# Kernel tuning notes

Measured on AMD Instinct MI355X. Metric: run time of the kernel, lower is better.

Reference implementation:

```python
import jax, jax.numpy as jnp
import numpy as np

MESSAGE_SIZE = 128
MESSAGE_PASSES = 3
N_BONDS = 7      # Single, Double, Triple, Quadruple, Aromatic, Pi, Universal
N_LAYERS = 8     # 8 bias-free Linear layers, ReLU after the first 7
N_TYPES = 6      # top-4 ranked atoms + atom 0, plus catchall slot (index 5)
ATOM_VALS = [6.0, 7.0, 8.0, 9.0, 16.0, 17.0, 1.0]
TOP_ATOMS = [6.0, 7.0, 8.0, 9.0, 0.0]


def setup_inputs() -> dict:
    key = jax.random.key(0)
    ks = jax.random.split(key, 8)
    B, N, F, D = 128, 128, 75, MESSAGE_SIZE
    g = jax.random.uniform(ks[0], (B, N_BONDS, N, N), dtype=jnp.float32)
    h = jax.random.normal(ks[1], (B, N, F), dtype=jnp.float32)
    # channel 0 carries the atomic number used for GRU routing
    atom_ids = jax.random.randint(ks[2], (B, N), 0, len(ATOM_VALS))
    h = h.at[:, :, 0].set(jnp.asarray(ATOM_VALS, jnp.float32)[atom_ids])
    s = 1.0 / np.sqrt(D)
    msg_W = jax.random.normal(ks[3], (N_BONDS, N_LAYERS, D, D), jnp.float32) * s
    gru_Wih = jax.random.normal(ks[4], (2, N_TYPES, 3 * D, D), jnp.float32) * s  # [regular/universal, type, 3H, H]
    gru_Whh = jax.random.normal(ks[5], (2, N_TYPES, 3 * D, D), jnp.float32) * s
    gru_bih = jax.random.normal(ks[6], (2, N_TYPES, 3 * D), jnp.float32) * s
    gru_bhh = jax.random.normal(ks[7], (2, N_TYPES, 3 * D), jnp.float32) * s
    return dict(g=g, h=h, msg_W=msg_W, gru_Wih=gru_Wih, gru_Whh=gru_Whh,
                gru_bih=gru_bih, gru_bhh=gru_bhh)


def _gru_grouped(x, hx, tid, Wih, Whh, bih, bhh):
    """torch.nn.GRUCell(input=x, hx=hx) with per-node parameter group tid in [0,T).
    Wih/Whh: [T, 3H, H], bih/bhh: [T, 3H]."""
    gx = jnp.einsum('nd,tgd->ntg', x, Wih)   # [n, T, 3H]
    gh = jnp.einsum('nd,tgd->ntg', hx, Whh)
    gx = jnp.take_along_axis(gx, tid[:, None, None], axis=1)[:, 0] + bih[tid]
    gh = jnp.take_along_axis(gh, tid[:, None, None], axis=1)[:, 0] + bhh[tid]
    xr, xz, xn = jnp.split(gx, 3, axis=-1)
    hr, hz, hn = jnp.split(gh, 3, axis=-1)
    r = jax.nn.sigmoid(xr + hr)
    z = jax.nn.sigmoid(xz + hz)
    n = jnp.tanh(xn + r * hn)
    return (1.0 - z) * n + z * hx


def reference(g, h, msg_W, gru_Wih, gru_Whh, gru_bih, gru_bhh):
    B, N, F = h.shape
    D = msg_W.shape[-1]
    h_t = jnp.concatenate([h, jnp.zeros((B, N, D - F), h.dtype)], axis=2)  # [B,N,D]
    atoms = h[:, :, 0].reshape(-1)
    tid = jnp.full(atoms.shape, N_TYPES - 1, jnp.int32)  # default catchall
    for i, a in enumerate(TOP_ATOMS):
        tid = jnp.where(atoms == jnp.float32(a), jnp.int32(i), tid)
    for _ in range(MESSAGE_PASSES):
        # per-bond-type 8-layer bias-free MLP, vectorized over the 7 bond types
        xb = jnp.broadcast_to(h_t[None], (N_BONDS, B, N, D))
        for l in range(N_LAYERS):
            xb = jnp.einsum('kbnd,ked->kbne', xb, msg_W[:, l])
            if l < N_LAYERS - 1:
                xb = jax.nn.relu(xb)
        # bmm aggregation per bond type: m_k = g[:,k] @ xb_k
        m_all = jnp.einsum('bknm,kbmd->kbnd', g, xb)
        m_non = m_all[:N_BONDS - 1].sum(0).reshape(-1, D)
        m_uni = m_all[N_BONDS - 1].reshape(-1, D)
        h_flat = h_t.reshape(-1, D)
        out = _gru_grouped(h_flat, m_non, tid, gru_Wih[0], gru_Whh[0], gru_bih[0], gru_bhh[0])
        out_u = _gru_grouped(h_flat, m_uni, tid, gru_Wih[1], gru_Whh[1], gru_bih[1], gru_bhh[1])
        h_t = (out + out_u).reshape(B, N, D)
    return h_t
```

## Files before the change

kernel.cpp:

```cpp
#include <hip/hip_runtime.h>
#include <math.h>

#define NBOND 7
#define NLAY 8
#define NTYPE 6
#define NNODES 16384
#define PX 136

typedef _Float16 half8 __attribute__((ext_vector_type(8)));
typedef _Float16 half4 __attribute__((ext_vector_type(4)));
typedef float floatx16 __attribute__((ext_vector_type(16)));

__device__ __forceinline__ float sig_(float x) { return 1.0f / (1.0f + __expf(-x)); }
__device__ __forceinline__ int drow_(int reg, int hi) { return (reg & 3) + 8 * (reg >> 2) + 4 * hi; }

__device__ __forceinline__ _Float16 hi_(float v) { return (_Float16)v; }
__device__ __forceinline__ _Float16 lo_(float v) { return (_Float16)(v - (float)(_Float16)v); }

__global__ void setup_kernel(const float* __restrict__ h, float* __restrict__ hT,
                             int* __restrict__ counts, int* __restrict__ bucket)
{
    int gid = blockIdx.x * 256 + threadIdx.x;
    int node = gid >> 7, d = gid & 127;
    hT[gid] = (d < 75) ? h[node * 75 + d] : 0.0f;
    if (gid < NNODES) {
        float a = h[gid * 75];
        int tt = 5;
        if      (a == 6.0f) tt = 0;
        else if (a == 7.0f) tt = 1;
        else if (a == 8.0f) tt = 2;
        else if (a == 9.0f) tt = 3;
        else if (a == 0.0f) tt = 4;
        int slot = atomicAdd(&counts[tt], 1);
        bucket[tt * NNODES + slot] = gid;
    }
}

__global__ void pack_msg_kernel(const float* __restrict__ msgW, _Float16* __restrict__ Wp)
{
    int idx = blockIdx.x * 256 + threadIdx.x;
    if (idx >= NBOND * NLAY * 16 * 128) return;
    int e  = idx & 127;
    int c  = (idx >> 7) & 15;
    int kl = idx >> 11;
    const float* src = msgW + ((size_t)kl * 128 + e) * 128 + c * 8;
    float4 u = *(const float4*)src;
    float4 v = *(const float4*)(src + 4);
    float av[8] = {u.x, u.y, u.z, u.w, v.x, v.y, v.z, v.w};
    half8 hh, ll;
    #pragma unroll
    for (int j = 0; j < 8; ++j) { hh[j] = hi_(av[j]); ll[j] = lo_(av[j]); }
    _Float16* dst = Wp + ((size_t)kl * 16 + c) * 2048;
    *(half8*)(dst + e * 8)        = hh;
    *(half8*)(dst + 1024 + e * 8) = ll;
}

__global__ void pack_gru_kernel(const float* __restrict__ Wih, const float* __restrict__ Whh,
                                _Float16* __restrict__ Wp)
{
    int idx = blockIdx.x * 256 + threadIdx.x;
    if (idx >= 2 * NTYPE * 2 * 16 * 384) return;
    int col = idx % 384;
    int c   = (idx / 384) & 15;
    int vm  = idx / 6144;
    int mat = vm & 1;
    int vt  = vm >> 1;
    const float* src = (mat ? Whh : Wih) + ((size_t)vt * 384 + col) * 128 + c * 8;
    float4 u = *(const float4*)src;
    float4 v = *(const float4*)(src + 4);
    float av[8] = {u.x, u.y, u.z, u.w, v.x, v.y, v.z, v.w};
    half8 hh, ll;
    #pragma unroll
    for (int j = 0; j < 8; ++j) { hh[j] = hi_(av[j]); ll[j] = lo_(av[j]); }
    _Float16* dst = Wp + (size_t)vm * 98304 + (size_t)c * 6144;
    *(half8*)(dst + col * 8)        = hh;
    *(half8*)(dst + 3072 + col * 8) = ll;
}

__global__ __launch_bounds__(512, 4) void mlp_agg_mfma(
    const float* __restrict__ hin, const _Float16* __restrict__ Wp,
    const float* __restrict__ gmat, float* __restrict__ m_non, float* __restrict__ m_uni)
{
    __shared__ _Float16 Xhi[128 * PX];
    __shared__ _Float16 Xlo[128 * PX];

    const int t = threadIdx.x;
    const int kb = blockIdx.x, b = blockIdx.y;
    const int wave = t >> 6, lane = t & 63, lo = lane & 31, hi = lane >> 5;
    const int ctw = wave & 3, rh = wave >> 2;
    const int wcol = ctw * 32 + lo;

    for (int q = t; q < 128 * 32; q += 512) {
        int r = q >> 5, c4 = q & 31;
        float4 v = *(const float4*)(hin + ((size_t)(b * 128 + r)) * 128 + c4 * 4);
        half4 hh, ll;
        hh[0] = hi_(v.x); ll[0] = lo_(v.x);
        hh[1] = hi_(v.y); ll[1] = lo_(v.y);
        hh[2] = hi_(v.z); ll[2] = lo_(v.z);
        hh[3] = hi_(v.w); ll[3] = lo_(v.w);
        *(half4*)(Xhi + r * PX + c4 * 4) = hh;
        *(half4*)(Xlo + r * PX + c4 * 4) = ll;
    }
    __syncthreads();

    floatx16 acc[2];

    #pragma unroll 1
    for (int l = 0; l < NLAY; ++l) {
        #pragma unroll
        for (int r2 = 0; r2 < 2; ++r2) acc[r2] = (floatx16)0.0f;
        const _Float16* wb = Wp + ((size_t)(kb * NLAY + l) * 16) * 2048;

        #pragma unroll
        for (int kk = 0; kk < 8; ++kk) {
            const _Float16* bp = wb + (size_t)(kk * 2 + hi) * 2048;
            half8 b_h = *(const half8*)(bp + wcol * 8);
            half8 b_l = *(const half8*)(bp + 1024 + wcol * 8);
            #pragma unroll
            for (int r2 = 0; r2 < 2; ++r2) {
                int rrow = (rh * 2 + r2) * 32 + lo;
                half8 a_h = *(const half8*)(Xhi + rrow * PX + kk * 16 + hi * 8);
                half8 a_l = *(const half8*)(Xlo + rrow * PX + kk * 16 + hi * 8);
                acc[r2] = __builtin_amdgcn_mfma_f32_32x32x16_f16(a_h, b_h, acc[r2], 0, 0, 0);
                acc[r2] = __builtin_amdgcn_mfma_f32_32x32x16_f16(a_h, b_l, acc[r2], 0, 0, 0);
                acc[r2] = __builtin_amdgcn_mfma_f32_32x32x16_f16(a_l, b_h, acc[r2], 0, 0, 0);
            }
        }
        __syncthreads();

        if (l < NLAY - 1) {
            #pragma unroll
            for (int r2 = 0; r2 < 2; ++r2)
                #pragma unroll
                for (int reg = 0; reg < 16; ++reg) {
                    int n = (rh * 2 + r2) * 32 + drow_(reg, hi);
                    float vv = fmaxf(acc[r2][reg], 0.0f);
                    Xhi[n * PX + wcol] = hi_(vv);
                    Xlo[n * PX + wcol] = lo_(vv);
                }
        } else {
            #pragma unroll
            for (int r2 = 0; r2 < 2; ++r2)
                #pragma unroll
                for (int s = 0; s < 4; ++s) {
                    int m0 = (rh * 2 + r2) * 32 + 8 * s + 4 * hi;
                    half4 hh, ll;
                    #pragma unroll
                    for (int j = 0; j < 4; ++j) {
                        float vv = acc[r2][4 * s + j];
                        hh[j] = hi_(vv); ll[j] = lo_(vv);
                    }
                    *(half4*)(Xhi + wcol * PX + m0) = hh;
                    *(half4*)(Xlo + wcol * PX + m0) = ll;
                }
        }
        __syncthreads();
    }

    const int rtw = wave & 3, ch = wave >> 2;
    const int row = rtw * 32 + lo;
    #pragma unroll
    for (int c2 = 0; c2 < 2; ++c2) acc[c2] = (floatx16)0.0f;
    const float* grow = gmat + (size_t)(b * NBOND + kb) * 16384;

    #pragma unroll 2
    for (int kk = 0; kk < 8; ++kk) {
        const float* gp = grow + (size_t)row * 128 + kk * 16 + hi * 8;
        float4 u = *(const float4*)gp, v2 = *(const float4*)(gp + 4);
        float av[8] = {u.x, u.y, u.z, u.w, v2.x, v2.y, v2.z, v2.w};
        half8 a_h, a_l;
        #pragma unroll
        for (int j = 0; j < 8; ++j) { a_h[j] = hi_(av[j]); a_l[j] = lo_(av[j]); }
        #pragma unroll
        for (int c2 = 0; c2 < 2; ++c2) {
            int ct = ch * 2 + c2;
            half8 b_h = *(const half8*)(Xhi + (ct * 32 + lo) * PX + kk * 16 + hi * 8);
            half8 b_l = *(const half8*)(Xlo + (ct * 32 + lo) * PX + kk * 16 + hi * 8);
            acc[c2] = __builtin_amdgcn_mfma_f32_32x32x16_f16(a_h, b_h, acc[c2], 0, 0, 0);
            acc[c2] = __builtin_amdgcn_mfma_f32_32x32x16_f16(a_h, b_l, acc[c2], 0, 0, 0);
            acc[c2] = __builtin_amdgcn_mfma_f32_32x32x16_f16(a_l, b_h, acc[c2], 0, 0, 0);
        }
    }

    if (kb == NBOND - 1) {
        #pragma unroll
        for (int c2 = 0; c2 < 2; ++c2)
            #pragma unroll
            for (int reg = 0; reg < 16; ++reg) {
                int n = rtw * 32 + drow_(reg, hi);
                m_uni[((size_t)(b * 128 + n)) * 128 + (ch * 2 + c2) * 32 + lo] = acc[c2][reg];
            }
    } else {
        #pragma unroll
        for (int c2 = 0; c2 < 2; ++c2)
            #pragma unroll
            for (int reg = 0; reg < 16; ++reg) {
                int n = rtw * 32 + drow_(reg, hi);
                atomicAdd(m_non + ((size_t)(b * 128 + n)) * 128 + (ch * 2 + c2) * 32 + lo,
                          acc[c2][reg]);
            }
    }
}

__global__ __launch_bounds__(256, 3) void gru_mfma(
    float* __restrict__ hT,
    const float* __restrict__ m_non, const float* __restrict__ m_uni,
    const int* __restrict__ counts, const int* __restrict__ bucket,
    const _Float16* __restrict__ Wp, const float* __restrict__ bihp, const float* __restrict__ bhhp)
{
    __shared__ _Float16 Xh[32 * PX], Xl[32 * PX], Mh[32 * PX], Ml[32 * PX];
    __shared__ int bl[32];

    const int t = threadIdx.x, tt = blockIdx.y, rtile = blockIdx.z;
    const int cnt  = counts[tt];
    const int base = blockIdx.x * 64 + rtile * 32;
    if (base >= cnt) return;
    const int nn = min(32, cnt - base);
    if (t < 32) bl[t] = (t < nn) ? bucket[tt * NNODES + base + t] : -1;
    __syncthreads();

    for (int q = t; q < 32 * 32; q += 256) {
        int r = q >> 5, c4 = q & 31;
        float4 xv = make_float4(0.f, 0.f, 0.f, 0.f);
        int node = bl[r];
        if (node >= 0) xv = *(const float4*)(hT + (size_t)node * 128 + c4 * 4);
        half4 hh, ll;
        hh[0] = hi_(xv.x); ll[0] = lo_(xv.x);
        hh[1] = hi_(xv.y); ll[1] = lo_(xv.y);
        hh[2] = hi_(xv.z); ll[2] = lo_(xv.z);
        hh[3] = hi_(xv.w); ll[3] = lo_(xv.w);
        *(half4*)(Xh + r * PX + c4 * 4) = hh;
        *(half4*)(Xl + r * PX + c4 * 4) = ll;
    }

    const int wave = t >> 6, lane = t & 63, lo = lane & 31, hi = lane >> 5;
    const int d = wave * 32 + lo;

    #pragma unroll 1
    for (int v = 0; v < 2; ++v) {
        const float* msrc = v ? m_uni : m_non;
        __syncthreads();
        for (int q = t; q < 32 * 32; q += 256) {
            int r = q >> 5, c4 = q & 31;
            float4 mv = make_float4(0.f, 0.f, 0.f, 0.f);
            int node = bl[r];
            if (node >= 0) mv = *(const float4*)(msrc + (size_t)node * 128 + c4 * 4);
            half4 hh, ll;
            hh[0] = hi_(mv.x); ll[0] = lo_(mv.x);
            hh[1] = hi_(mv.y); ll[1] = lo_(mv.y);
            hh[2] = hi_(mv.z); ll[2] = lo_(mv.z);
            hh[3] = hi_(mv.w); ll[3] = lo_(mv.w);
            *(half4*)(Mh + r * PX + c4 * 4) = hh;
            *(half4*)(Ml + r * PX + c4 * 4) = ll;
        }
        __syncthreads();

        const int vt = v * NTYPE + tt;
        const _Float16* pih = Wp + (size_t)(vt * 2 + 0) * 98304;
        const _Float16* phh = Wp + (size_t)(vt * 2 + 1) * 98304;

        floatx16 ar = (floatx16)0.0f, az = (floatx16)0.0f;
        floatx16 ax = (floatx16)0.0f, ah = (floatx16)0.0f;

        #pragma unroll 2
        for (int kk = 0; kk < 8; ++kk) {
            int koff = kk * 16 + hi * 8;
            half8 xh = *(const half8*)(Xh + lo * PX + koff);
            half8 xl = *(const half8*)(Xl + lo * PX + koff);
            half8 mh = *(const half8*)(Mh + lo * PX + koff);
            half8 ml = *(const half8*)(Ml + lo * PX + koff);
            const _Float16* ci = pih + (size_t)(kk * 2 + hi) * 6144;
            const _Float16* ch = phh + (size_t)(kk * 2 + hi) * 6144;
            half8 birh = *(const half8*)(ci + (0   + d) * 8);
            half8 birl = *(const half8*)(ci + 3072 + (0   + d) * 8);
            half8 bizh = *(const half8*)(ci + (128 + d) * 8);
            half8 bizl = *(const half8*)(ci + 3072 + (128 + d) * 8);
            half8 binh = *(const half8*)(ci + (256 + d) * 8);
            half8 binl = *(const half8*)(ci + 3072 + (256 + d) * 8);
            half8 bhrh = *(const half8*)(ch + (0   + d) * 8);
            half8 bhrl = *(const half8*)(ch + 3072 + (0   + d) * 8);
            half8 bhzh = *(const half8*)(ch + (128 + d) * 8);
            half8 bhzl = *(const half8*)(ch + 3072 + (128 + d) * 8);
            half8 bhnh = *(const half8*)(ch + (256 + d) * 8);
            half8 bhnl = *(const half8*)(ch + 3072 + (256 + d) * 8);

            ar = __builtin_amdgcn_mfma_f32_32x32x16_f16(xh, birh, ar, 0, 0, 0);
            ar = __builtin_amdgcn_mfma_f32_32x32x16_f16(xh, birl, ar, 0, 0, 0);
            ar = __builtin_amdgcn_mfma_f32_32x32x16_f16(xl, birh, ar, 0, 0, 0);
            ar = __builtin_amdgcn_mfma_f32_32x32x16_f16(mh, bhrh, ar, 0, 0, 0);
            ar = __builtin_amdgcn_mfma_f32_32x32x16_f16(mh, bhrl, ar, 0, 0, 0);
            ar = __builtin_amdgcn_mfma_f32_32x32x16_f16(ml, bhrh, ar, 0, 0, 0);

            az = __builtin_amdgcn_mfma_f32_32x32x16_f16(xh, bizh, az, 0, 0, 0);
            az = __builtin_amdgcn_mfma_f32_32x32x16_f16(xh, bizl, az, 0, 0, 0);
            az = __builtin_amdgcn_mfma_f32_32x32x16_f16(xl, bizh, az, 0, 0, 0);
            az = __builtin_amdgcn_mfma_f32_32x32x16_f16(mh, bhzh, az, 0, 0, 0);
            az = __builtin_amdgcn_mfma_f32_32x32x16_f16(mh, bhzl, az, 0, 0, 0);
            az = __builtin_amdgcn_mfma_f32_32x32x16_f16(ml, bhzh, az, 0, 0, 0);

            ax = __builtin_amdgcn_mfma_f32_32x32x16_f16(xh, binh, ax, 0, 0, 0);
            ax = __builtin_amdgcn_mfma_f32_32x32x16_f16(xh, binl, ax, 0, 0, 0);
            ax = __builtin_amdgcn_mfma_f32_32x32x16_f16(xl, binh, ax, 0, 0, 0);
            ah = __builtin_amdgcn_mfma_f32_32x32x16_f16(mh, bhnh, ah, 0, 0, 0);
            ah = __builtin_amdgcn_mfma_f32_32x32x16_f16(mh, bhnl, ah, 0, 0, 0);
            ah = __builtin_amdgcn_mfma_f32_32x32x16_f16(ml, bhnh, ah, 0, 0, 0);
        }

        const float* bi = bihp + (size_t)vt * 384;
        const float* bh = bhhp + (size_t)vt * 384;
        float b_r  = bi[d] + bh[d];
        float b_z  = bi[128 + d] + bh[128 + d];
        float b_in = bi[256 + d];
        float b_hn = bh[256 + d];
        #pragma unroll
        for (int reg = 0; reg < 16; ++reg) {
            int n = drow_(reg, hi);
            int node = bl[n];
            if (node < 0) continue;
            float r  = sig_(ar[reg] + b_r);
            float z  = sig_(az[reg] + b_z);
            float nv = tanhf(ax[reg] + b_in + r * (ah[reg] + b_hn));
            float mv = msrc[(size_t)node * 128 + d];
            float val = (1.0f - z) * nv + z * mv;
            if (v == 0) hT[(size_t)node * 128 + d] = val;
            else        hT[(size_t)node * 128 + d] += val;
        }
    }
}

extern "C" void kernel_launch(void* const* d_in, const int* in_sizes, int n_in,
                              void* d_out, int out_size, void* d_ws, size_t ws_size,
                              hipStream_t stream) {
    const float* g    = (const float*)d_in[0];
    const float* h    = (const float*)d_in[1];
    const float* msgW = (const float*)d_in[2];
    const float* Wih  = (const float*)d_in[3];
    const float* Whh  = (const float*)d_in[4];
    const float* bih  = (const float*)d_in[5];
    const float* bhh  = (const float*)d_in[6];
    float* hT = (float*)d_out;

    char* ws = (char*)d_ws;
    float* m_non = (float*)ws;
    float* m_uni = m_non + (size_t)NNODES * 128;
    int* counts  = (int*)(ws + 2 * (size_t)NNODES * 128 * 4);
    int* bucket  = counts + 8;
    _Float16* WpM = (_Float16*)(bucket + NTYPE * NNODES);
    _Float16* WpG = WpM + (size_t)NBOND * NLAY * 16 * 2048;

    (void)hipMemsetAsync(counts, 0, 8 * sizeof(int), stream);
    setup_kernel<<<NNODES * 128 / 256, 256, 0, stream>>>(h, hT, counts, bucket);
    pack_msg_kernel<<<(NBOND * NLAY * 16 * 128 + 255) / 256, 256, 0, stream>>>(msgW, WpM);
    pack_gru_kernel<<<(2 * NTYPE * 2 * 16 * 384 + 255) / 256, 256, 0, stream>>>(Wih, Whh, WpG);

    for (int pass = 0; pass < 3; ++pass) {
        (void)hipMemsetAsync(m_non, 0, (size_t)NNODES * 128 * 4, stream);
        mlp_agg_mfma<<<dim3(NBOND, 128), 512, 0, stream>>>(hT, WpM, g, m_non, m_uni);
        gru_mfma<<<dim3(NNODES / 64, NTYPE, 2), 256, 0, stream>>>(hT, m_non, m_uni, counts, bucket,
                                                                  WpG, bih, bhh);
    }
}
```

Baseline: 778.8 us.

## Prefetch next-layer weights and aggregation matrix into registers during MFMA loops

Weights for the next MLP layer are loaded from global memory into registers while the current layer's activations are written back, and the adjacency-matrix rows are prefetched during the last layer. The aim is to hide global load latency behind LDS writeback and barriers. The first sync of each layer is replaced by a raw s_barrier with scheduling barriers, relying on the LDS reads in the MFMA loop being complete before activations are overwritten. Register pressure rises considerably (16 half8 plus 16 float4), which may cause spills or lower occupancy under launch_bounds(512,4).

New measurement: 1.500 ms. 1.93x slower.

```diff
diff --git a/kernel.cpp b/kernel.cpp
--- a/kernel.cpp
+++ b/kernel.cpp
@@ -89,6 +89,24 @@
     const int wave = t >> 6, lane = t & 63, lo = lane & 31, hi = lane >> 5;
     const int ctw = wave & 3, rh = wave >> 2;
     const int wcol = ctw * 32 + lo;
+    const int rtw = wave & 3, ch = wave >> 2;
+    const int aggrow = rtw * 32 + lo;
+    const float* grow = gmat + (size_t)(b * NBOND + kb) * 16384;
+
+    half8 Wh[8], Wl[8];
+    float4 greg[16];
+    floatx16 acc[2];
+
+    {
+        const _Float16* wb0 = Wp + ((size_t)(kb * NLAY) * 16) * 2048;
+        #pragma unroll
+        for (int kk = 0; kk < 8; ++kk) {
+            const _Float16* bp = wb0 + (size_t)(kk * 2 + hi) * 2048;
+            Wh[kk] = *(const half8*)(bp + wcol * 8);
+            Wl[kk] = *(const half8*)(bp + 1024 + wcol * 8);
+        }
+    }
+    __builtin_amdgcn_sched_barrier(0);
 
     for (int q = t; q < 128 * 32; q += 512) {
         int r = q >> 5, c4 = q & 31;
@@ -103,30 +121,44 @@
     }
     __syncthreads();
 
-    floatx16 acc[2];
-
     #pragma unroll 1
     for (int l = 0; l < NLAY; ++l) {
         #pragma unroll
         for (int r2 = 0; r2 < 2; ++r2) acc[r2] = (floatx16)0.0f;
-        const _Float16* wb = Wp + ((size_t)(kb * NLAY + l) * 16) * 2048;
 
         #pragma unroll
         for (int kk = 0; kk < 8; ++kk) {
-            const _Float16* bp = wb + (size_t)(kk * 2 + hi) * 2048;
-            half8 b_h = *(const half8*)(bp + wcol * 8);
-            half8 b_l = *(const half8*)(bp + 1024 + wcol * 8);
             #pragma unroll
             for (int r2 = 0; r2 < 2; ++r2) {
                 int rrow = (rh * 2 + r2) * 32 + lo;
                 half8 a_h = *(const half8*)(Xhi + rrow * PX + kk * 16 + hi * 8);
                 half8 a_l = *(const half8*)(Xlo + rrow * PX + kk * 16 + hi * 8);
-                acc[r2] = __builtin_amdgcn_mfma_f32_32x32x16_f16(a_h, b_h, acc[r2], 0, 0, 0);
-                acc[r2] = __builtin_amdgcn_mfma_f32_32x32x16_f16(a_h, b_l, acc[r2], 0, 0, 0);
-                acc[r2] = __builtin_amdgcn_mfma_f32_32x32x16_f16(a_l, b_h, acc[r2], 0, 0, 0);
-            }
-        }
-        __syncthreads();
+                acc[r2] = __builtin_amdgcn_mfma_f32_32x32x16_f16(a_h, Wh[kk], acc[r2], 0, 0, 0);
+                acc[r2] = __builtin_amdgcn_mfma_f32_32x32x16_f16(a_h, Wl[kk], acc[r2], 0, 0, 0);
+                acc[r2] = __builtin_amdgcn_mfma_f32_32x32x16_f16(a_l, Wh[kk], acc[r2], 0, 0, 0);
+            }
+        }
+
+        if (l < NLAY - 1) {
+            const _Float16* wbn = Wp + ((size_t)(kb * NLAY + l + 1) * 16) * 2048;
+            #pragma unroll
+            for (int kk = 0; kk < 8; ++kk) {
+                const _Float16* bp = wbn + (size_t)(kk * 2 + hi) * 2048;
+                Wh[kk] = *(const half8*)(bp + wcol * 8);
+                Wl[kk] = *(const half8*)(bp + 1024 + wcol * 8);
+            }
+        } else {
+            #pragma unroll
+            for (int k2 = 0; k2 < 8; ++k2) {
+                const float* gp = grow + (size_t)aggrow * 128 + k2 * 16 + hi * 8;
+                greg[k2 * 2]     = *(const float4*)gp;
+                greg[k2 * 2 + 1] = *(const float4*)(gp + 4);
+            }
+        }
+        __builtin_amdgcn_sched_barrier(0);
+
+        asm volatile("" ::: "memory");
+        __builtin_amdgcn_s_barrier();
 
         if (l < NLAY - 1) {
             #pragma unroll
@@ -154,19 +186,19 @@
                     *(half4*)(Xlo + wcol * PX + m0) = ll;
                 }
         }
-        __syncthreads();
-    }
-
-    const int rtw = wave & 3, ch = wave >> 2;
-    const int row = rtw * 32 + lo;
+
+        asm volatile("s_waitcnt lgkmcnt(0)" ::: "memory");
+        __builtin_amdgcn_s_barrier();
+        asm volatile("" ::: "memory");
+        __builtin_amdgcn_sched_barrier(0);
+    }
+
     #pragma unroll
     for (int c2 = 0; c2 < 2; ++c2) acc[c2] = (floatx16)0.0f;
-    const float* grow = gmat + (size_t)(b * NBOND + kb) * 16384;
-
-    #pragma unroll 2
+
+    #pragma unroll
     for (int kk = 0; kk < 8; ++kk) {
-        const float* gp = grow + (size_t)row * 128 + kk * 16 + hi * 8;
-        float4 u = *(const float4*)gp, v2 = *(const float4*)(gp + 4);
+        float4 u = greg[kk * 2], v2 = greg[kk * 2 + 1];
         float av[8] = {u.x, u.y, u.z, u.w, v2.x, v2.y, v2.z, v2.w};
         half8 a_h, a_l;
         #pragma unroll
```

## Stage MLP weights into LDS with async double-buffered global_load_lds

Applied to the files above, without the earlier changes.

The per-layer weight fragments are now copied into shared memory with async global-to-LDS loads, split in two halves. Each half for the next layer is prefetched while the current layer computes, using explicit vmcnt waits and raw barriers in place of __syncthreads. This removes the direct global loads of B operands from the MFMA loop. In exchange, LDS use grows by 64 KB, the launch bound drops from 4 to 2 blocks per CU, and correctness depends on hand-placed waitcnt and barrier ordering.

Result: slower. 880.9 us (+13.1%).

```diff
diff --git a/kernel.cpp b/kernel.cpp
--- a/kernel.cpp
+++ b/kernel.cpp
@@ -6,6 +6,7 @@
 #define NTYPE 6
 #define NNODES 16384
 #define PX 136
+#define WCH 2048
 
 typedef _Float16 half8 __attribute__((ext_vector_type(8)));
 typedef _Float16 half4 __attribute__((ext_vector_type(4)));
@@ -50,7 +51,7 @@
     half8 hh, ll;
     #pragma unroll
     for (int j = 0; j < 8; ++j) { hh[j] = hi_(av[j]); ll[j] = lo_(av[j]); }
-    _Float16* dst = Wp + ((size_t)kl * 16 + c) * 2048;
+    _Float16* dst = Wp + ((size_t)kl * 16 + c) * WCH;
     *(half8*)(dst + e * 8)        = hh;
     *(half8*)(dst + 1024 + e * 8) = ll;
 }
@@ -77,18 +78,35 @@
     *(half8*)(dst + 3072 + col * 8) = ll;
 }
 
-__global__ __launch_bounds__(512, 4) void mlp_agg_mfma(
+__global__ __launch_bounds__(512, 2) void mlp_agg_mfma(
     const float* __restrict__ hin, const _Float16* __restrict__ Wp,
     const float* __restrict__ gmat, float* __restrict__ m_non, float* __restrict__ m_uni)
 {
     __shared__ _Float16 Xhi[128 * PX];
     __shared__ _Float16 Xlo[128 * PX];
+    __shared__ _Float16 Wb[2][8 * WCH];
 
     const int t = threadIdx.x;
     const int kb = blockIdx.x, b = blockIdx.y;
     const int wave = t >> 6, lane = t & 63, lo = lane & 31, hi = lane >> 5;
     const int ctw = wave & 3, rh = wave >> 2;
     const int wcol = ctw * 32 + lo;
+
+    const _Float16* wlay = Wp + ((size_t)(kb * NLAY) * 16) * WCH;
+
+    auto stageW = [&](int l, int hfl) {
+        const _Float16* src = wlay + ((size_t)l * 16 + hfl * 8) * WCH + wave * 2048 + lane * 8;
+        _Float16* dst = &Wb[hfl][wave * 2048];
+        #pragma unroll
+        for (int i = 0; i < 4; ++i) {
+            __builtin_amdgcn_global_load_lds(
+                (const __attribute__((address_space(1))) void*)(src + i * 512),
+                (__attribute__((address_space(3))) void*)(dst + i * 512), 16, 0, 0);
+        }
+    };
+
+    stageW(0, 0);
+    stageW(0, 1);
 
     for (int q = t; q < 128 * 32; q += 512) {
         int r = q >> 5, c4 = q & 31;
@@ -109,13 +127,12 @@
     for (int l = 0; l < NLAY; ++l) {
         #pragma unroll
         for (int r2 = 0; r2 < 2; ++r2) acc[r2] = (floatx16)0.0f;
-        const _Float16* wb = Wp + ((size_t)(kb * NLAY + l) * 16) * 2048;
-
-        #pragma unroll
-        for (int kk = 0; kk < 8; ++kk) {
-            const _Float16* bp = wb + (size_t)(kk * 2 + hi) * 2048;
-            half8 b_h = *(const half8*)(bp + wcol * 8);
-            half8 b_l = *(const half8*)(bp + 1024 + wcol * 8);
+
+        #pragma unroll
+        for (int kk = 0; kk < 4; ++kk) {
+            const _Float16* wp = &Wb[0][(kk * 2 + hi) * WCH];
+            half8 b_h = *(const half8*)(wp + wcol * 8);
+            half8 b_l = *(const half8*)(wp + 1024 + wcol * 8);
             #pragma unroll
             for (int r2 = 0; r2 < 2; ++r2) {
                 int rrow = (rh * 2 + r2) * 32 + lo;
@@ -126,7 +143,37 @@
                 acc[r2] = __builtin_amdgcn_mfma_f32_32x32x16_f16(a_l, b_h, acc[r2], 0, 0, 0);
             }
         }
-        __syncthreads();
+        asm volatile("" ::: "memory");
+        __builtin_amdgcn_s_barrier();
+
+        if (l < NLAY - 1) {
+            stageW(l + 1, 0);
+            asm volatile("s_waitcnt vmcnt(4)" ::: "memory");
+        } else {
+            asm volatile("s_waitcnt vmcnt(0)" ::: "memory");
+        }
+        __builtin_amdgcn_sched_barrier(0);
+        __builtin_amdgcn_s_barrier();
+
+        #pragma unroll
+        for (int kk = 4; kk < 8; ++kk) {
+            const _Float16* wp = &Wb[1][((kk - 4) * 2 + hi) * WCH];
+            half8 b_h = *(const half8*)(wp + wcol * 8);
+            half8 b_l = *(const half8*)(wp + 1024 + wcol * 8);
+            #pragma unroll
+            for (int r2 = 0; r2 < 2; ++r2) {
+                int rrow = (rh * 2 + r2) * 32 + lo;
+                half8 a_h = *(const half8*)(Xhi + rrow * PX + kk * 16 + hi * 8);
+                half8 a_l = *(const half8*)(Xlo + rrow * PX + kk * 16 + hi * 8);
+                acc[r2] = __builtin_amdgcn_mfma_f32_32x32x16_f16(a_h, b_h, acc[r2], 0, 0, 0);
+                acc[r2] = __builtin_amdgcn_mfma_f32_32x32x16_f16(a_h, b_l, acc[r2], 0, 0, 0);
+                acc[r2] = __builtin_amdgcn_mfma_f32_32x32x16_f16(a_l, b_h, acc[r2], 0, 0, 0);
+            }
+        }
+        asm volatile("" ::: "memory");
+        __builtin_amdgcn_s_barrier();
+
+        if (l < NLAY - 1) stageW(l + 1, 1);
 
         if (l < NLAY - 1) {
             #pragma unroll
@@ -138,6 +185,7 @@
                     Xhi[n * PX + wcol] = hi_(vv);
                     Xlo[n * PX + wcol] = lo_(vv);
                 }
+            asm volatile("s_waitcnt vmcnt(4) lgkmcnt(0)" ::: "memory");
         } else {
             #pragma unroll
             for (int r2 = 0; r2 < 2; ++r2)
@@ -153,8 +201,10 @@
                     *(half4*)(Xhi + wcol * PX + m0) = hh;
                     *(half4*)(Xlo + wcol * PX + m0) = ll;
                 }
-        }
-        __syncthreads();
+            asm volatile("s_waitcnt lgkmcnt(0)" ::: "memory");
+        }
+        __builtin_amdgcn_sched_barrier(0);
+        __builtin_amdgcn_s_barrier();
     }
 
     const int rtw = wave & 3, ch = wave >> 2;
@@ -346,7 +396,7 @@
     int* counts  = (int*)(ws + 2 * (size_t)NNODES * 128 * 4);
     int* bucket  = counts + 8;
     _Float16* WpM = (_Float16*)(bucket + NTYPE * NNODES);
-    _Float16* WpG = WpM + (size_t)NBOND * NLAY * 16 * 2048;
+    _Float16* WpG = WpM + (size_t)NBOND * NLAY * 16 * WCH;
 
     (void)hipMemsetAsync(counts, 0, 8 * sizeof(int), stream);
     setup_kernel<<<NNODES * 128 / 256, 256, 0, stream>>>(h, hT, counts, bucket);
```
